# Performance work log

Measured on AMD Instinct MI355X. Metric: run time of the kernel, lower is better.

## Reference

```python
import jax, jax.numpy as jnp
import numpy as np

B, N, C, DIN, DOUT = 16, 65536, 256, 16, 16  # ratio = N // C = 256 nodes per cluster


def setup_inputs() -> dict:
    key = jax.random.key(0)
    k1, k2, k3, k4, k5 = jax.random.split(key, 5)
    stdv = 1.0 / np.sqrt(DOUT)
    x = jax.random.normal(k1, (B, N, DIN), dtype=jnp.float32)
    # parameters, pre-reshaped: torch w_diag (in*out, C) with out-major io axis -> (out, in, C)
    w_diag = jax.random.uniform(k2, (DOUT, DIN, C), jnp.float32, -stdv, stdv)
    w_off = jax.random.uniform(k3, (DOUT, DIN, C, C), jnp.float32, -stdv, stdv)
    b1 = jax.random.uniform(k4, (DOUT,), jnp.float32, -stdv, stdv)
    # flatten_ids(cluster_ids): a permutation putting each cluster's nodes contiguous
    permute_ids = jax.random.permutation(k5, N)
    return {"x": x, "w_diag": w_diag, "w_off": w_off, "b1": b1, "permute_ids": permute_ids}


def reference(x, w_diag, w_off, b1, permute_ids):
    # Faithful to: W = rearrange(kron(diag_embed(w_diag), I_r)) + (1/N) rearrange(kron(w_off, 1_{rxr}))
    # out = inv_permute( reshape( W @ flatten(permute(x)) ) ) + b1,
    # computed via the block-constant structure instead of materializing the (Dout*N, Din*N) W.
    Bq, Nn, Din = x.shape
    Dout, _, Cc = w_diag.shape
    ratio = Nn // Cc
    inv_permute = jnp.argsort(permute_ids)
    xp = x[:, permute_ids, :]                       # (B, N, Din), cluster-contiguous
    xc = xp.reshape(Bq, Cc, ratio, Din)             # (B, C, r, Din)
    # diagonal blocks: per-cluster Din->Dout mixing, identity over within-cluster index
    out_diag = jnp.einsum('oic,bcri->bcro', w_diag, xc)   # (B, C, r, Dout)
    # off blocks: constant within each (cluster j, cluster k) block -> use cluster sums
    s = xc.sum(axis=2)                              # (B, C, Din)
    out_off = jnp.einsum('oick,bki->bco', w_off, s) / Nn  # (B, C, Dout)
    out = out_diag + out_off[:, :, None, :]         # broadcast over within-cluster index
    out = out.reshape(Bq, Nn, Dout)[:, inv_permute, :] + b1[None, None, :]
    return out
```

## Files before the change

### kernel.cpp

```cpp
#include <hip/hip_runtime.h>

#define B_    16
#define N_    65536
#define C_    256
#define DIN_  16
#define DOUT_ 16
#define RATIO_ 256


__global__ __launch_bounds__(256) void k_prep(
    const float* __restrict__ w_diag, const int* __restrict__ P,
    float* __restrict__ wd_t, int* __restrict__ c_of_n)
{
    int t = threadIdx.x;
    int bid = blockIdx.x;
    if (bid < 256) {
        int o = bid >> 4, i = bid & 15;
        float v = w_diag[(o * DIN_ + i) * C_ + t];
        wd_t[t * 256 + i * 16 + o] = v;
    } else {
        int k = bid - 256;
        int j = k * 256 + t;
        c_of_n[P[j]] = k;
    }
}

__global__ __launch_bounds__(256) void k_main(
    const float* __restrict__ x, const int* __restrict__ P,
    const float* __restrict__ wd_t, float* __restrict__ s,
    float* __restrict__ out)
{
    int bid = blockIdx.x;
    int b = bid >> 8, k = bid & (C_ - 1);
    int t = threadIdx.x;
    __shared__ float4 wds[64];
    __shared__ float4 part[4][4];

    reinterpret_cast<float*>(wds)[t] = wd_t[k * 256 + t];

    int n = P[(k << 8) + t];
    const float4* row =
        reinterpret_cast<const float4*>(x + ((size_t)(b * N_ + n)) * DIN_);
    float4 x0 = row[0], x1 = row[1], x2 = row[2], x3 = row[3];
    __syncthreads();

    float xv[16];
    xv[0]=x0.x; xv[1]=x0.y; xv[2]=x0.z; xv[3]=x0.w;
    xv[4]=x1.x; xv[5]=x1.y; xv[6]=x1.z; xv[7]=x1.w;
    xv[8]=x2.x; xv[9]=x2.y; xv[10]=x2.z; xv[11]=x2.w;
    xv[12]=x3.x; xv[13]=x3.y; xv[14]=x3.z; xv[15]=x3.w;

    float4 a0 = make_float4(0.f,0.f,0.f,0.f), a1 = a0, a2 = a0, a3 = a0;
    #pragma unroll
    for (int i = 0; i < 16; ++i) {
        float xi = xv[i];
        float4 w0 = wds[i * 4 + 0];
        float4 w1 = wds[i * 4 + 1];
        float4 w2 = wds[i * 4 + 2];
        float4 w3 = wds[i * 4 + 3];
        a0.x += xi * w0.x; a0.y += xi * w0.y; a0.z += xi * w0.z; a0.w += xi * w0.w;
        a1.x += xi * w1.x; a1.y += xi * w1.y; a1.z += xi * w1.z; a1.w += xi * w1.w;
        a2.x += xi * w2.x; a2.y += xi * w2.y; a2.z += xi * w2.z; a2.w += xi * w2.w;
        a3.x += xi * w3.x; a3.y += xi * w3.y; a3.z += xi * w3.z; a3.w += xi * w3.w;
    }
    float4* orow =
        reinterpret_cast<float4*>(out + ((size_t)(b * N_ + n)) * DOUT_);
    orow[0] = a0; orow[1] = a1; orow[2] = a2; orow[3] = a3;

    #pragma unroll
    for (int mask = 1; mask <= 2; mask <<= 1) {
        x0.x += __shfl_xor(x0.x, mask, 64); x0.y += __shfl_xor(x0.y, mask, 64);
        x0.z += __shfl_xor(x0.z, mask, 64); x0.w += __shfl_xor(x0.w, mask, 64);
        x1.x += __shfl_xor(x1.x, mask, 64); x1.y += __shfl_xor(x1.y, mask, 64);
        x1.z += __shfl_xor(x1.z, mask, 64); x1.w += __shfl_xor(x1.w, mask, 64);
        x2.x += __shfl_xor(x2.x, mask, 64); x2.y += __shfl_xor(x2.y, mask, 64);
        x2.z += __shfl_xor(x2.z, mask, 64); x2.w += __shfl_xor(x2.w, mask, 64);
        x3.x += __shfl_xor(x3.x, mask, 64); x3.y += __shfl_xor(x3.y, mask, 64);
        x3.z += __shfl_xor(x3.z, mask, 64); x3.w += __shfl_xor(x3.w, mask, 64);
    }
    int q = t & 3;
    float4 v = (q == 0) ? x0 : (q == 1) ? x1 : (q == 2) ? x2 : x3;
    #pragma unroll
    for (int mask = 4; mask <= 32; mask <<= 1) {
        v.x += __shfl_xor(v.x, mask, 64);
        v.y += __shfl_xor(v.y, mask, 64);
        v.z += __shfl_xor(v.z, mask, 64);
        v.w += __shfl_xor(v.w, mask, 64);
    }
    int lane = t & 63, wave = t >> 6;
    if (lane < 4) part[wave][lane] = v;
    __syncthreads();
    if (t < 16) {
        int qq = t >> 2, comp = t & 3;
        float sv = 0.f;
        #pragma unroll
        for (int w = 0; w < 4; ++w) {
            const float* p = reinterpret_cast<const float*>(&part[w][qq]);
            sv += p[comp];
        }
        int i = qq * 4 + comp;
        s[i * (B_ * C_) + b * C_ + k] = sv;
    }
}

__global__ __launch_bounds__(256) void k_off(
    const float* __restrict__ w_off, const float* __restrict__ s,
    const float* __restrict__ b1, float* __restrict__ off)
{
    int c  = blockIdx.x >> 2;
    int og = blockIdx.x & 3;
    int t  = threadIdx.x;
    float acc[64];
    #pragma unroll
    for (int z = 0; z < 64; ++z) acc[z] = 0.f;

    for (int i = 0; i < DIN_; ++i) {
        float wv[4];
        #pragma unroll
        for (int o4 = 0; o4 < 4; ++o4) {
            int o = og * 4 + o4;
            wv[o4] = w_off[((size_t)((o * DIN_ + i) * C_ + c)) * C_ + t];
        }
        #pragma unroll
        for (int b = 0; b < B_; ++b) {
            float sv = s[i * (B_ * C_) + b * C_ + t];
            #pragma unroll
            for (int o4 = 0; o4 < 4; ++o4) acc[b * 4 + o4] += wv[o4] * sv;
        }
    }

    __shared__ float red[8][256];
    const float invN = 1.0f / (float)N_;
    #pragma unroll
    for (int rd = 0; rd < 8; ++rd) {
        __syncthreads();
        #pragma unroll
        for (int oo = 0; oo < 8; ++oo) red[oo][t] = acc[rd * 8 + oo];
        __syncthreads();
        int grp = t >> 5;
        int seg = t & 31;
        float p = 0.f;
        #pragma unroll
        for (int j = 0; j < 8; ++j) p += red[grp][seg * 8 + j];
        #pragma unroll
        for (int d = 16; d > 0; d >>= 1) p += __shfl_down(p, d, 32);
        if (seg == 0) {
            int outid = rd * 8 + grp;
            int b  = outid >> 2, o4 = outid & 3;
            int o  = og * 4 + o4;
            off[((b << 8) + c) * DOUT_ + o] = p * invN + b1[o];
        }
    }
}

__global__ __launch_bounds__(256) void k_add_off(
    const int* __restrict__ c_of_n, const float* __restrict__ off,
    float* __restrict__ out)
{
    size_t g = (size_t)blockIdx.x * 256 + threadIdx.x;
    int rowid = (int)(g >> 2);
    int b = rowid >> 16;
    int n = rowid & 65535;
    int q = (int)(g & 3);
    int c = c_of_n[n];
    const float4* offp =
        reinterpret_cast<const float4*>(off + (size_t)(((b << 8) + c) * DOUT_));
    float4 o4 = offp[q];
    float4* op = reinterpret_cast<float4*>(out) + g;
    float4 v = *op;
    v.x += o4.x; v.y += o4.y; v.z += o4.z; v.w += o4.w;
    *op = v;
}

extern "C" void kernel_launch(void* const* d_in, const int* in_sizes, int n_in,
                              void* d_out, int out_size, void* d_ws, size_t ws_size,
                              hipStream_t stream) {
    const float* x      = (const float*)d_in[0];
    const float* w_diag = (const float*)d_in[1];
    const float* w_off  = (const float*)d_in[2];
    const float* b1     = (const float*)d_in[3];
    const int*   P      = (const int*)d_in[4];
    float* out    = (float*)d_out;
    float* s      = (float*)d_ws;
    float* off    = s + 65536;
    float* wd_t   = off + 65536;
    int*   c_of_n = (int*)(wd_t + 65536);

    k_prep<<<512, 256, 0, stream>>>(w_diag, P, wd_t, c_of_n);
    k_main<<<B_ * C_, 256, 0, stream>>>(x, P, wd_t, s, out);
    k_off<<<C_ * 4, 256, 0, stream>>>(w_off, s, b1, off);
    k_add_off<<<(B_ * N_ * DOUT_ / 4) / 256, 256, 0, stream>>>(c_of_n, off, out);
}
```

Before: 226.6 us.

## Stream x sequentially for cluster sums and fuse diagonal transform with offset add

Replaces the gather-based main kernel with two streaming passes. The first reads x in node order and accumulates per-cluster sums with LDS atomics, then flushes them to global memory with global atomics into a buffer zeroed in the prep kernel. The second reads x again in order and computes the diagonal mix plus the precomputed cluster offset in one pass, writing the output once instead of writing it and then reading and rewriting it in a separate add kernel. This trades the random-row gathers and the extra output read-modify-write for a second sequential read of x and contended LDS atomics.

```diff
diff --git a/kernel.cpp b/kernel.cpp
--- a/kernel.cpp
+++ b/kernel.cpp
@@ -5,101 +5,57 @@
 #define C_    256
 #define DIN_  16
 #define DOUT_ 16
-#define RATIO_ 256
 
 
 __global__ __launch_bounds__(256) void k_prep(
     const float* __restrict__ w_diag, const int* __restrict__ P,
-    float* __restrict__ wd_t, int* __restrict__ c_of_n)
+    float* __restrict__ wd_t, int* __restrict__ c_of_n,
+    float* __restrict__ s)
 {
     int t = threadIdx.x;
     int bid = blockIdx.x;
     if (bid < 256) {
         int o = bid >> 4, i = bid & 15;
-        float v = w_diag[(o * DIN_ + i) * C_ + t];
+        float v = w_diag[bid * C_ + t];
         wd_t[t * 256 + i * 16 + o] = v;
     } else {
         int k = bid - 256;
-        int j = k * 256 + t;
-        c_of_n[P[j]] = k;
+        c_of_n[P[k * 256 + t]] = k;
+        s[k * 256 + t] = 0.f;
     }
 }
 
-__global__ __launch_bounds__(256) void k_main(
-    const float* __restrict__ x, const int* __restrict__ P,
-    const float* __restrict__ wd_t, float* __restrict__ s,
-    float* __restrict__ out)
+__global__ __launch_bounds__(256) void k_sum(
+    const float* __restrict__ x, const int* __restrict__ c_of_n,
+    float* __restrict__ s)
 {
+    __shared__ float lds[C_ * 17];
+    int t = threadIdx.x;
     int bid = blockIdx.x;
-    int b = bid >> 8, k = bid & (C_ - 1);
-    int t = threadIdx.x;
-    __shared__ float4 wds[64];
-    __shared__ float4 part[4][4];
-
-    reinterpret_cast<float*>(wds)[t] = wd_t[k * 256 + t];
-
-    int n = P[(k << 8) + t];
-    const float4* row =
-        reinterpret_cast<const float4*>(x + ((size_t)(b * N_ + n)) * DIN_);
-    float4 x0 = row[0], x1 = row[1], x2 = row[2], x3 = row[3];
+    int b = bid >> 5, slab = bid & 31;
+    #pragma unroll
+    for (int m = 0; m < 17; ++m) lds[m * 256 + t] = 0.f;
     __syncthreads();
 
-    float xv[16];
-    xv[0]=x0.x; xv[1]=x0.y; xv[2]=x0.z; xv[3]=x0.w;
-    xv[4]=x1.x; xv[5]=x1.y; xv[6]=x1.z; xv[7]=x1.w;
-    xv[8]=x2.x; xv[9]=x2.y; xv[10]=x2.z; xv[11]=x2.w;
-    xv[12]=x3.x; xv[13]=x3.y; xv[14]=x3.z; xv[15]=x3.w;
-
-    float4 a0 = make_float4(0.f,0.f,0.f,0.f), a1 = a0, a2 = a0, a3 = a0;
+    int lr = t >> 2, q = t & 3;
+    const float4* x4 = reinterpret_cast<const float4*>(x);
+    int row0 = slab * 2048;
+    #pragma unroll 2
+    for (int m = 0; m < 32; ++m) {
+        int r = row0 + m * 64 + lr;
+        float4 v = x4[((size_t)(b * N_ + r)) * 4 + q];
+        int c = c_of_n[r];
+        float* dst = &lds[c * 17 + q * 4];
+        atomicAdd(dst + 0, v.x);
+        atomicAdd(dst + 1, v.y);
+        atomicAdd(dst + 2, v.z);
+        atomicAdd(dst + 3, v.w);
+    }
+    __syncthreads();
     #pragma unroll
     for (int i = 0; i < 16; ++i) {
-        float xi = xv[i];
-        float4 w0 = wds[i * 4 + 0];
-        float4 w1 = wds[i * 4 + 1];
-        float4 w2 = wds[i * 4 + 2];
-        float4 w3 = wds[i * 4 + 3];
-        a0.x += xi * w0.x; a0.y += xi * w0.y; a0.z += xi * w0.z; a0.w += xi * w0.w;
-        a1.x += xi * w1.x; a1.y += xi * w1.y; a1.z += xi * w1.z; a1.w += xi * w1.w;
-        a2.x += xi * w2.x; a2.y += xi * w2.y; a2.z += xi * w2.z; a2.w += xi * w2.w;
-        a3.x += xi * w3.x; a3.y += xi * w3.y; a3.z += xi * w3.z; a3.w += xi * w3.w;
-    }
-    float4* orow =
-        reinterpret_cast<float4*>(out + ((size_t)(b * N_ + n)) * DOUT_);
-    orow[0] = a0; orow[1] = a1; orow[2] = a2; orow[3] = a3;
-
-    #pragma unroll
-    for (int mask = 1; mask <= 2; mask <<= 1) {
-        x0.x += __shfl_xor(x0.x, mask, 64); x0.y += __shfl_xor(x0.y, mask, 64);
-        x0.z += __shfl_xor(x0.z, mask, 64); x0.w += __shfl_xor(x0.w, mask, 64);
-        x1.x += __shfl_xor(x1.x, mask, 64); x1.y += __shfl_xor(x1.y, mask, 64);
-        x1.z += __shfl_xor(x1.z, mask, 64); x1.w += __shfl_xor(x1.w, mask, 64);
-        x2.x += __shfl_xor(x2.x, mask, 64); x2.y += __shfl_xor(x2.y, mask, 64);
-        x2.z += __shfl_xor(x2.z, mask, 64); x2.w += __shfl_xor(x2.w, mask, 64);
-        x3.x += __shfl_xor(x3.x, mask, 64); x3.y += __shfl_xor(x3.y, mask, 64);
-        x3.z += __shfl_xor(x3.z, mask, 64); x3.w += __shfl_xor(x3.w, mask, 64);
-    }
-    int q = t & 3;
-    float4 v = (q == 0) ? x0 : (q == 1) ? x1 : (q == 2) ? x2 : x3;
-    #pragma unroll
-    for (int mask = 4; mask <= 32; mask <<= 1) {
-        v.x += __shfl_xor(v.x, mask, 64);
-        v.y += __shfl_xor(v.y, mask, 64);
-        v.z += __shfl_xor(v.z, mask, 64);
-        v.w += __shfl_xor(v.w, mask, 64);
-    }
-    int lane = t & 63, wave = t >> 6;
-    if (lane < 4) part[wave][lane] = v;
-    __syncthreads();
-    if (t < 16) {
-        int qq = t >> 2, comp = t & 3;
-        float sv = 0.f;
-        #pragma unroll
-        for (int w = 0; w < 4; ++w) {
-            const float* p = reinterpret_cast<const float*>(&part[w][qq]);
-            sv += p[comp];
-        }
-        int i = qq * 4 + comp;
-        s[i * (B_ * C_) + b * C_ + k] = sv;
+        float v = lds[t * 17 + i];
+        unsafeAtomicAdd(&s[i * (B_ * C_) + b * C_ + t], v);
     }
 }
 
@@ -153,23 +109,47 @@
     }
 }
 
-__global__ __launch_bounds__(256) void k_add_off(
-    const int* __restrict__ c_of_n, const float* __restrict__ off,
+__global__ __launch_bounds__(256) void k_apply_seq(
+    const float* __restrict__ x, const int* __restrict__ c_of_n,
+    const float* __restrict__ wd_t, const float* __restrict__ off,
     float* __restrict__ out)
 {
-    size_t g = (size_t)blockIdx.x * 256 + threadIdx.x;
-    int rowid = (int)(g >> 2);
-    int b = rowid >> 16;
-    int n = rowid & 65535;
-    int q = (int)(g & 3);
+    int t = threadIdx.x;
+    int lr = t >> 2, q = t & 3;
+    int n = blockIdx.x * 64 + lr;
     int c = c_of_n[n];
-    const float4* offp =
-        reinterpret_cast<const float4*>(off + (size_t)(((b << 8) + c) * DOUT_));
-    float4 o4 = offp[q];
-    float4* op = reinterpret_cast<float4*>(out) + g;
-    float4 v = *op;
-    v.x += o4.x; v.y += o4.y; v.z += o4.z; v.w += o4.w;
-    *op = v;
+
+    const float4* wd4 = reinterpret_cast<const float4*>(wd_t);
+    float4 wds[16];
+    #pragma unroll
+    for (int i = 0; i < 16; ++i) wds[i] = wd4[c * 64 + i * 4 + q];
+
+    const float4* x4   = reinterpret_cast<const float4*>(x);
+    const float4* off4 = reinterpret_cast<const float4*>(off);
+    float4* out4       = reinterpret_cast<float4*>(out);
+
+    #pragma unroll 2
+    for (int b = 0; b < B_; ++b) {
+        size_t rowbase = ((size_t)(b * N_ + n)) * 4;
+        float4 x0 = x4[rowbase + 0];
+        float4 x1 = x4[rowbase + 1];
+        float4 x2 = x4[rowbase + 2];
+        float4 x3 = x4[rowbase + 3];
+        float4 acc = off4[((size_t)((b << 8) + c)) * 4 + q];
+        float xv[16];
+        xv[0]=x0.x; xv[1]=x0.y; xv[2]=x0.z; xv[3]=x0.w;
+        xv[4]=x1.x; xv[5]=x1.y; xv[6]=x1.z; xv[7]=x1.w;
+        xv[8]=x2.x; xv[9]=x2.y; xv[10]=x2.z; xv[11]=x2.w;
+        xv[12]=x3.x; xv[13]=x3.y; xv[14]=x3.z; xv[15]=x3.w;
+        #pragma unroll
+        for (int i = 0; i < 16; ++i) {
+            acc.x += xv[i] * wds[i].x;
+            acc.y += xv[i] * wds[i].y;
+            acc.z += xv[i] * wds[i].z;
+            acc.w += xv[i] * wds[i].w;
+        }
+        out4[rowbase + q] = acc;
+    }
 }
 
 extern "C" void kernel_launch(void* const* d_in, const int* in_sizes, int n_in,
@@ -186,8 +166,8 @@
     float* wd_t   = off + 65536;
     int*   c_of_n = (int*)(wd_t + 65536);
 
-    k_prep<<<512, 256, 0, stream>>>(w_diag, P, wd_t, c_of_n);
-    k_main<<<B_ * C_, 256, 0, stream>>>(x, P, wd_t, s, out);
+    k_prep<<<512, 256, 0, stream>>>(w_diag, P, wd_t, c_of_n, s);
+    k_sum<<<512, 256, 0, stream>>>(x, c_of_n, s);
     k_off<<<C_ * 4, 256, 0, stream>>>(w_off, s, b1, off);
-    k_add_off<<<(B_ * N_ * DOUT_ / 4) / 256, 256, 0, stream>>>(c_of_n, off, out);
+    k_apply_seq<<<N_ / 64, 256, 0, stream>>>(x, c_of_n, wd_t, off, out);
 }
```

Result: slower. 279.0 us (+23.1%).
